# Performance work log

Hardware: AMD Instinct MI355X
Metric: run time of the kernel (lower is better)

The kernel has to match this reference:

```python
import jax, jax.numpy as jnp
import numpy as np

BATCH_SIZE = 8192   # args.batch_size
NUM_VIEWS = 2       # args.num_views
TEMPERATURE = 0.07  # args.loss_args['temperature']
FEAT_DIM = 256
N = (BATCH_SIZE // 2) * NUM_VIEWS  # rows of features


def _static_index_maps():
    # labels = sorted cat of num_views copies of arange(batch_size//2)
    labels = np.sort(np.tile(np.arange(BATCH_SIZE // 2), NUM_VIEWS))
    lab_mat = labels[None, :] == labels[:, None]          # (N, N) bool
    # off-diagonal column indices: for row i, columns [0..N-1] excluding i,
    # in ascending order (matches torch boolean-mask extraction order)
    j = np.arange(N - 1)
    cols = j[None, :] + (j[None, :] >= np.arange(N)[:, None])  # (N, N-1)
    lab_off = np.take_along_axis(lab_mat, cols, axis=1)        # (N, N-1) bool
    k = NUM_VIEWS - 1  # positives per row
    # stable sort puts positive positions first, preserving column order
    order = np.argsort(~lab_off, axis=1, kind='stable')
    pos_cols = order[:, :k]   # (N, k)
    neg_cols = order[:, k:]   # (N, N-1-k)
    return cols, pos_cols, neg_cols

_COLS, _POS_COLS, _NEG_COLS = _static_index_maps()


def setup_inputs() -> dict:
    key = jax.random.key(0)
    features = jax.random.normal(key, (N, FEAT_DIM), dtype=jnp.float32)
    return {"features": features}


def reference(features):
    # L2 normalize rows (F.normalize eps clamp)
    norm = jnp.maximum(jnp.linalg.norm(features, axis=1, keepdims=True), 1e-12)
    f = features / norm
    sim = f @ f.T                                            # (N, N)
    sim_off = jnp.take_along_axis(sim, jnp.asarray(_COLS), axis=1)       # (N, N-1)
    positives = jnp.take_along_axis(sim_off, jnp.asarray(_POS_COLS), axis=1)
    negatives = jnp.take_along_axis(sim_off, jnp.asarray(_NEG_COLS), axis=1)
    logits = jnp.concatenate([positives, negatives], axis=1) / TEMPERATURE
    # CrossEntropyLoss with target class 0 for every row
    loss = jnp.mean(-jax.nn.log_softmax(logits, axis=1)[:, 0])
    return loss
```

## Files before the change

### kernel.cpp

```cpp
#include <hip/hip_runtime.h>
#include <stdint.h>

#define N_ROWS 8192
#define FEAT   256
#define YSPLIT 16
#define CPB    (N_ROWS / YSPLIT)
#define CT     64
#define LDS_STRIDE 264

typedef __bf16 bf16x8 __attribute__((ext_vector_type(8)));
typedef float  f32x4  __attribute__((ext_vector_type(4)));

__device__ __forceinline__ unsigned short f2bf(float x) {
    union { float f; uint32_t u; } v; v.f = x;
    uint32_t u = v.u;
    return (unsigned short)((u + 0x7FFFu + ((u >> 16) & 1u)) >> 16);
}

__global__ void knorm(const float* __restrict__ feat,
                      unsigned short* __restrict__ fb,
                      float* __restrict__ pos) {
    __shared__ float ex[4][FEAT];
    int wave = threadIdx.x >> 6;
    int lane = threadIdx.x & 63;
    int row  = blockIdx.x * 4 + wave;
    float4 v = ((const float4*)(feat + row * FEAT))[lane];
    float ss = v.x*v.x + v.y*v.y + v.z*v.z + v.w*v.w;
    #pragma unroll
    for (int off = 1; off < 64; off <<= 1) ss += __shfl_xor(ss, off);
    float inv = 1.0f / fmaxf(sqrtf(ss), 1e-12f);
    float4 o; o.x = v.x*inv; o.y = v.y*inv; o.z = v.z*inv; o.w = v.w*inv;
    ushort4 b;
    b.x = f2bf(o.x); b.y = f2bf(o.y); b.z = f2bf(o.z); b.w = f2bf(o.w);
    ((ushort4*)(fb + row * FEAT))[lane] = b;
    ((float4*)ex[wave])[lane] = o;
    __syncthreads();
    float4 p = ((float4*)ex[wave ^ 1])[lane];
    float d = o.x*p.x + o.y*p.y + o.z*p.z + o.w*p.w;
    #pragma unroll
    for (int off = 1; off < 64; off <<= 1) d += __shfl_xor(d, off);
    if (lane == 0) pos[row] = d;
}

__global__ __launch_bounds__(512)
void kmain(const unsigned short* __restrict__ fb, float* __restrict__ partial) {
    __shared__ unsigned short Bs[CT][LDS_STRIDE];
    const int t    = threadIdx.x;
    const int lane = t & 63;
    const int wave = t >> 6;
    const int quad = lane >> 4;
    const int l15  = lane & 15;
    const int rw    = blockIdx.x * 256 + wave * 32;
    const int cbase = blockIdx.y * CPB;
    const float Kc = 20.60992915555662f;

    bf16x8 af[2][8];
    #pragma unroll
    for (int rf = 0; rf < 2; ++rf)
        #pragma unroll
        for (int ks = 0; ks < 8; ++ks) {
            int row = rw + rf * 16 + l15;
            int k   = ks * 32 + quad * 8;
            af[rf][ks] = *(const bf16x8*)(fb + row * FEAT + k);
        }

    float lsum[2][4] = {{0.f,0.f,0.f,0.f},{0.f,0.f,0.f,0.f}};

    for (int ct = 0; ct < CPB / CT; ++ct) {
        __syncthreads();
        const int c0 = cbase + ct * CT;
        #pragma unroll
        for (int i = 0; i < 4; ++i) {
            int idx = t + i * 512;
            int r = idx >> 5;
            int o = (idx & 31) * 8;
            *(uint4*)(&Bs[r][o]) = *(const uint4*)(fb + (c0 + r) * FEAT + o);
        }
        __syncthreads();

        #pragma unroll
        for (int g = 0; g < 4; ++g) {
            const int cg = c0 + g * 16;
            f32x4 acc0 = {0.f,0.f,0.f,0.f};
            f32x4 acc1 = {0.f,0.f,0.f,0.f};
            #pragma unroll
            for (int ks = 0; ks < 8; ++ks) {
                bf16x8 b = *(const bf16x8*)(&Bs[g * 16 + l15][ks * 32 + quad * 8]);
                acc0 = __builtin_amdgcn_mfma_f32_16x16x32_bf16(af[0][ks], b, acc0, 0, 0, 0);
                acc1 = __builtin_amdgcn_mfma_f32_16x16x32_bf16(af[1][ks], b, acc1, 0, 0, 0);
            }
            const bool dg = (cg < rw + 32) && (cg + 16 > rw);
            const int C = cg + l15;
            #pragma unroll
            for (int r = 0; r < 4; ++r) {
                float e0 = __builtin_amdgcn_exp2f(fmaf(acc0[r], Kc, -Kc));
                float e1 = __builtin_amdgcn_exp2f(fmaf(acc1[r], Kc, -Kc));
                if (dg) {
                    int R0 = rw + quad * 4 + r;
                    if (R0 == C)      e0 = 0.f;
                    if (R0 + 16 == C) e1 = 0.f;
                }
                lsum[0][r] += e0;
                lsum[1][r] += e1;
            }
        }
    }

    #pragma unroll
    for (int rf = 0; rf < 2; ++rf)
        #pragma unroll
        for (int r = 0; r < 4; ++r) {
            float v = lsum[rf][r];
            v += __shfl_xor(v, 1);
            v += __shfl_xor(v, 2);
            v += __shfl_xor(v, 4);
            v += __shfl_xor(v, 8);
            lsum[rf][r] = v;
        }
    if (l15 == 0) {
        #pragma unroll
        for (int rf = 0; rf < 2; ++rf)
            #pragma unroll
            for (int r = 0; r < 4; ++r) {
                int row = rw + rf * 16 + quad * 4 + r;
                partial[blockIdx.y * N_ROWS + row] = lsum[rf][r];
            }
    }
}

__global__ void kreduce(const float* __restrict__ partial,
                        const float* __restrict__ pos,
                        float* __restrict__ bsum) {
    __shared__ float red[4];
    int row  = blockIdx.x * 256 + threadIdx.x;
    int wave = threadIdx.x >> 6;
    int lane = threadIdx.x & 63;
    float L = 0.f;
    #pragma unroll
    for (int p = 0; p < YSPLIT; ++p) L += partial[p * N_ROWS + row];
    const float invT = 14.285714285714286f;
    float loss = invT * (1.0f - pos[row])
               + 0.6931471805599453f * __builtin_amdgcn_logf(L);
    #pragma unroll
    for (int off = 1; off < 64; off <<= 1) loss += __shfl_xor(loss, off);
    if (lane == 0) red[wave] = loss;
    __syncthreads();
    if (threadIdx.x == 0)
        bsum[blockIdx.x] = red[0] + red[1] + red[2] + red[3];
}

__global__ void kfinal(const float* __restrict__ bsum, float* __restrict__ out) {
    int lane = threadIdx.x;
    float v = (lane < 32) ? bsum[lane] : 0.f;
    #pragma unroll
    for (int off = 1; off < 32; off <<= 1) v += __shfl_xor(v, off);
    if (lane == 0) out[0] = v * (1.0f / 8192.0f);
}

extern "C" void kernel_launch(void* const* d_in, const int* in_sizes, int n_in,
                              void* d_out, int out_size, void* d_ws, size_t ws_size,
                              hipStream_t stream) {
    const float* feat = (const float*)d_in[0];
    float* out = (float*)d_out;
    char* ws = (char*)d_ws;
    unsigned short* fb      = (unsigned short*)ws;
    float*          partial = (float*)(ws + (4u << 20));
    float*          pos     = (float*)(ws + (4u << 20) + (1u << 19));
    float*          bsum    = (float*)(ws + (4u << 20) + (1u << 19) + (1u << 15));

    knorm<<<N_ROWS / 4, 256, 0, stream>>>(feat, fb, pos);
    kmain<<<dim3(32, YSPLIT), 512, 0, stream>>>(fb, partial);
    kreduce<<<N_ROWS / 256, 256, 0, stream>>>(partial, pos, bsum);
    kfinal<<<1, 64, 0, stream>>>(bsum, out);
}
```

Before: 104.8 us.

## Double-buffer B tiles via direct global-to-LDS loads with swizzled layout

The main kernel now stages column tiles straight from global memory into LDS with global_load_lds, using two buffers so the next tile loads while the current one is computed. The normalize kernel writes bf16 rows in an XOR-swizzled chunk order, which lets the unpadded LDS tile avoid bank conflicts. Each wave now handles 64 rows instead of 32, with 256 threads per block and launch bounds requesting two blocks per CU, so each LDS B fragment feeds four MFMAs. This costs more registers for the A fragments and accumulators, and the LDS footprint doubles.

After: 125.4 us. 19.7% more time.

```diff
diff --git a/kernel.cpp b/kernel.cpp
--- a/kernel.cpp
+++ b/kernel.cpp
@@ -6,7 +6,6 @@
 #define YSPLIT 16
 #define CPB    (N_ROWS / YSPLIT)
 #define CT     64
-#define LDS_STRIDE 264
 
 typedef __bf16 bf16x8 __attribute__((ext_vector_type(8)));
 typedef float  f32x4  __attribute__((ext_vector_type(4)));
@@ -15,6 +14,12 @@
     union { float f; uint32_t u; } v; v.f = x;
     uint32_t u = v.u;
     return (unsigned short)((u + 0x7FFFu + ((u >> 16) & 1u)) >> 16);
+}
+
+__device__ __forceinline__ void gld16(const unsigned short* g, unsigned short* l) {
+    __builtin_amdgcn_global_load_lds((__attribute__((address_space(1))) void*)g,
+                                     (__attribute__((address_space(3))) void*)l,
+                                     16, 0, 0);
 }
 
 __global__ void knorm(const float* __restrict__ feat,
@@ -32,7 +37,8 @@
     float4 o; o.x = v.x*inv; o.y = v.y*inv; o.z = v.z*inv; o.w = v.w*inv;
     ushort4 b;
     b.x = f2bf(o.x); b.y = f2bf(o.y); b.z = f2bf(o.z); b.w = f2bf(o.w);
-    ((ushort4*)(fb + row * FEAT))[lane] = b;
+    int sidx = (((lane >> 1) ^ (row & 7)) << 1) | (lane & 1);
+    ((ushort4*)(fb + row * FEAT))[sidx] = b;
     ((float4*)ex[wave])[lane] = o;
     __syncthreads();
     float4 p = ((float4*)ex[wave ^ 1])[lane];
@@ -42,72 +48,90 @@
     if (lane == 0) pos[row] = d;
 }
 
-__global__ __launch_bounds__(512)
+__global__ __launch_bounds__(256, 2)
 void kmain(const unsigned short* __restrict__ fb, float* __restrict__ partial) {
-    __shared__ unsigned short Bs[CT][LDS_STRIDE];
+    __shared__ unsigned short bufA[CT * FEAT];
+    __shared__ unsigned short bufB[CT * FEAT];
     const int t    = threadIdx.x;
     const int lane = t & 63;
     const int wave = t >> 6;
     const int quad = lane >> 4;
     const int l15  = lane & 15;
-    const int rw    = blockIdx.x * 256 + wave * 32;
+    const int rw    = blockIdx.x * 256 + wave * 64;
     const int cbase = blockIdx.y * CPB;
     const float Kc = 20.60992915555662f;
 
-    bf16x8 af[2][8];
-    #pragma unroll
-    for (int rf = 0; rf < 2; ++rf)
+#define STAGE(DST, CC0) do {                                                  \
+    const unsigned short* sp_ = fb + (size_t)(cbase + (CC0)) * FEAT + t * 8;  \
+    unsigned short* dp_ = (DST) + t * 8;                                      \
+    _Pragma("unroll")                                                         \
+    for (int i_ = 0; i_ < 8; ++i_)                                            \
+        gld16(sp_ + i_ * 2048, dp_ + i_ * 2048);                              \
+} while (0)
+
+    STAGE(bufA, 0);
+
+    bf16x8 af[4][8];
+    #pragma unroll
+    for (int rf = 0; rf < 4; ++rf)
         #pragma unroll
         for (int ks = 0; ks < 8; ++ks) {
             int row = rw + rf * 16 + l15;
-            int k   = ks * 32 + quad * 8;
-            af[rf][ks] = *(const bf16x8*)(fb + row * FEAT + k);
+            int ch  = (ks * 4 + quad) ^ (row & 7);
+            af[rf][ks] = *(const bf16x8*)(fb + row * FEAT + ch * 8);
         }
 
-    float lsum[2][4] = {{0.f,0.f,0.f,0.f},{0.f,0.f,0.f,0.f}};
-
-    for (int ct = 0; ct < CPB / CT; ++ct) {
-        __syncthreads();
-        const int c0 = cbase + ct * CT;
-        #pragma unroll
-        for (int i = 0; i < 4; ++i) {
-            int idx = t + i * 512;
-            int r = idx >> 5;
-            int o = (idx & 31) * 8;
-            *(uint4*)(&Bs[r][o]) = *(const uint4*)(fb + (c0 + r) * FEAT + o);
-        }
-        __syncthreads();
-
-        #pragma unroll
-        for (int g = 0; g < 4; ++g) {
-            const int cg = c0 + g * 16;
-            f32x4 acc0 = {0.f,0.f,0.f,0.f};
-            f32x4 acc1 = {0.f,0.f,0.f,0.f};
-            #pragma unroll
-            for (int ks = 0; ks < 8; ++ks) {
-                bf16x8 b = *(const bf16x8*)(&Bs[g * 16 + l15][ks * 32 + quad * 8]);
-                acc0 = __builtin_amdgcn_mfma_f32_16x16x32_bf16(af[0][ks], b, acc0, 0, 0, 0);
-                acc1 = __builtin_amdgcn_mfma_f32_16x16x32_bf16(af[1][ks], b, acc1, 0, 0, 0);
-            }
-            const bool dg = (cg < rw + 32) && (cg + 16 > rw);
-            const int C = cg + l15;
-            #pragma unroll
-            for (int r = 0; r < 4; ++r) {
-                float e0 = __builtin_amdgcn_exp2f(fmaf(acc0[r], Kc, -Kc));
-                float e1 = __builtin_amdgcn_exp2f(fmaf(acc1[r], Kc, -Kc));
-                if (dg) {
-                    int R0 = rw + quad * 4 + r;
-                    if (R0 == C)      e0 = 0.f;
-                    if (R0 + 16 == C) e1 = 0.f;
-                }
-                lsum[0][r] += e0;
-                lsum[1][r] += e1;
-            }
-        }
+    float lsum[4][4] = {{0.f,0.f,0.f,0.f},{0.f,0.f,0.f,0.f},
+                        {0.f,0.f,0.f,0.f},{0.f,0.f,0.f,0.f}};
+
+#define EPI(AC, RF) do {                                                      \
+    const int rb_ = rw + (RF) * 16;                                           \
+    const bool dg_ = (cg == rb_);          \
+    _Pragma("unroll")                                                         \
+    for (int r_ = 0; r_ < 4; ++r_) {                                          \
+        float e_ = __builtin_amdgcn_exp2f(fmaf((AC)[r_], Kc, -Kc));           \
+        if (dg_ && (rb_ + quad * 4 + r_ == C)) e_ = 0.f;     \
+        lsum[(RF)][r_] += e_;                                                 \
+    }                                                                         \
+} while (0)
+
+#define COMPUTE(BS, CC0) do {                                                 \
+    _Pragma("unroll")                                                         \
+    for (int g = 0; g < 4; ++g) {                                             \
+        const int cg = cbase + (CC0) + g * 16;                                \
+        const int C  = cg + l15;                                              \
+        f32x4 ac0 = {0.f,0.f,0.f,0.f};                                        \
+        f32x4 ac1 = {0.f,0.f,0.f,0.f};                                        \
+        f32x4 ac2 = {0.f,0.f,0.f,0.f};                                        \
+        f32x4 ac3 = {0.f,0.f,0.f,0.f};                                        \
+        _Pragma("unroll")                                                     \
+        for (int ks = 0; ks < 8; ++ks) {                                      \
+            bf16x8 b = *(const bf16x8*)((BS) + (g * 16 + l15) * FEAT          \
+                                        + (((ks * 4 + quad) ^ (l15 & 7)) * 8)); \
+            ac0 = __builtin_amdgcn_mfma_f32_16x16x32_bf16(af[0][ks], b, ac0, 0, 0, 0); \
+            ac1 = __builtin_amdgcn_mfma_f32_16x16x32_bf16(af[1][ks], b, ac1, 0, 0, 0); \
+            ac2 = __builtin_amdgcn_mfma_f32_16x16x32_bf16(af[2][ks], b, ac2, 0, 0, 0); \
+            ac3 = __builtin_amdgcn_mfma_f32_16x16x32_bf16(af[3][ks], b, ac3, 0, 0, 0); \
+        }                                                                     \
+        EPI(ac0, 0); EPI(ac1, 1); EPI(ac2, 2); EPI(ac3, 3);                   \
+    }                                                                         \
+} while (0)
+
+    asm volatile("s_waitcnt vmcnt(0)" ::: "memory");
+    __builtin_amdgcn_s_barrier();
+    for (int ct2 = 0; ct2 < CPB / CT; ct2 += 2) {
+        STAGE(bufB, (ct2 + 1) * CT);
+        COMPUTE(bufA, ct2 * CT);
+        asm volatile("s_waitcnt vmcnt(0)" ::: "memory");
+        __builtin_amdgcn_s_barrier();
+        if (ct2 + 2 < CPB / CT) STAGE(bufA, (ct2 + 2) * CT);
+        COMPUTE(bufB, (ct2 + 1) * CT);
+        asm volatile("s_waitcnt vmcnt(0)" ::: "memory");
+        __builtin_amdgcn_s_barrier();
     }
 
     #pragma unroll
-    for (int rf = 0; rf < 2; ++rf)
+    for (int rf = 0; rf < 4; ++rf)
         #pragma unroll
         for (int r = 0; r < 4; ++r) {
             float v = lsum[rf][r];
@@ -119,13 +143,16 @@
         }
     if (l15 == 0) {
         #pragma unroll
-        for (int rf = 0; rf < 2; ++rf)
+        for (int rf = 0; rf < 4; ++rf)
             #pragma unroll
             for (int r = 0; r < 4; ++r) {
                 int row = rw + rf * 16 + quad * 4 + r;
                 partial[blockIdx.y * N_ROWS + row] = lsum[rf][r];
             }
     }
+#undef STAGE
+#undef COMPUTE
+#undef EPI
 }
 
 __global__ void kreduce(const float* __restrict__ partial,
@@ -169,7 +196,7 @@
     float*          bsum    = (float*)(ws + (4u << 20) + (1u << 19) + (1u << 15));
 
     knorm<<<N_ROWS / 4, 256, 0, stream>>>(feat, fb, pos);
-    kmain<<<dim3(32, YSPLIT), 512, 0, stream>>>(fb, partial);
+    kmain<<<dim3(32, YSPLIT), 256, 0, stream>>>(fb, partial);
     kreduce<<<N_ROWS / 256, 256, 0, stream>>>(partial, pos, bsum);
     kfinal<<<1, 64, 0, stream>>>(bsum, out);
 }
```

## Drop LDS staging; read B fragments directly from swizzled global bf16 layout

Applied to the files above, without the earlier changes.

The normalize kernel now writes bf16 rows with an XOR swizzle of 16-byte chunks keyed by row. The main kernel drops the shared-memory tile and its barriers and loads B fragments straight from global memory or L2 using the matching swizzle. Each wave now covers 64 rows instead of 32, with 4 accumulators per B load, and blocks shrink to 256 threads. This removes LDS traffic and synchronisation and reuses each B fragment twice as much. The cost is higher register pressure, lower occupancy, and exposed global-load latency.

After: 106.0 us. Within noise of the previous version (+1.2%).

```diff
diff --git a/kernel.cpp b/kernel.cpp
--- a/kernel.cpp
+++ b/kernel.cpp
@@ -5,8 +5,6 @@
 #define FEAT   256
 #define YSPLIT 16
 #define CPB    (N_ROWS / YSPLIT)
-#define CT     64
-#define LDS_STRIDE 264
 
 typedef __bf16 bf16x8 __attribute__((ext_vector_type(8)));
 typedef float  f32x4  __attribute__((ext_vector_type(4)));
@@ -32,7 +30,8 @@
     float4 o; o.x = v.x*inv; o.y = v.y*inv; o.z = v.z*inv; o.w = v.w*inv;
     ushort4 b;
     b.x = f2bf(o.x); b.y = f2bf(o.y); b.z = f2bf(o.z); b.w = f2bf(o.w);
-    ((ushort4*)(fb + row * FEAT))[lane] = b;
+    int sidx = (((lane >> 1) ^ (row & 7)) << 1) | (lane & 1);
+    ((ushort4*)(fb + row * FEAT))[sidx] = b;
     ((float4*)ex[wave])[lane] = o;
     __syncthreads();
     float4 p = ((float4*)ex[wave ^ 1])[lane];
@@ -42,72 +41,64 @@
     if (lane == 0) pos[row] = d;
 }
 
-__global__ __launch_bounds__(512)
+__global__ __launch_bounds__(256, 1)
 void kmain(const unsigned short* __restrict__ fb, float* __restrict__ partial) {
-    __shared__ unsigned short Bs[CT][LDS_STRIDE];
     const int t    = threadIdx.x;
     const int lane = t & 63;
     const int wave = t >> 6;
     const int quad = lane >> 4;
     const int l15  = lane & 15;
-    const int rw    = blockIdx.x * 256 + wave * 32;
+    const int rw    = blockIdx.x * 256 + wave * 64;
     const int cbase = blockIdx.y * CPB;
     const float Kc = 20.60992915555662f;
 
-    bf16x8 af[2][8];
+    bf16x8 af[4][8];
     #pragma unroll
-    for (int rf = 0; rf < 2; ++rf)
+    for (int rf = 0; rf < 4; ++rf)
         #pragma unroll
         for (int ks = 0; ks < 8; ++ks) {
             int row = rw + rf * 16 + l15;
-            int k   = ks * 32 + quad * 8;
-            af[rf][ks] = *(const bf16x8*)(fb + row * FEAT + k);
+            int ch  = (ks * 4 + quad) ^ (row & 7);
+            af[rf][ks] = *(const bf16x8*)(fb + row * FEAT + ch * 8);
         }
 
-    float lsum[2][4] = {{0.f,0.f,0.f,0.f},{0.f,0.f,0.f,0.f}};
+    float lsum[4][4] = {{0.f,0.f,0.f,0.f},{0.f,0.f,0.f,0.f},
+                        {0.f,0.f,0.f,0.f},{0.f,0.f,0.f,0.f}};
 
-    for (int ct = 0; ct < CPB / CT; ++ct) {
-        __syncthreads();
-        const int c0 = cbase + ct * CT;
+    #pragma unroll 2
+    for (int g = 0; g < CPB / 16; ++g) {
+        const int cg = cbase + g * 16;
+        const int C  = cg + l15;
+        const unsigned short* bp = fb + (size_t)(cg + l15) * FEAT;
+        f32x4 ac0 = {0.f,0.f,0.f,0.f};
+        f32x4 ac1 = {0.f,0.f,0.f,0.f};
+        f32x4 ac2 = {0.f,0.f,0.f,0.f};
+        f32x4 ac3 = {0.f,0.f,0.f,0.f};
         #pragma unroll
-        for (int i = 0; i < 4; ++i) {
-            int idx = t + i * 512;
-            int r = idx >> 5;
-            int o = (idx & 31) * 8;
-            *(uint4*)(&Bs[r][o]) = *(const uint4*)(fb + (c0 + r) * FEAT + o);
+        for (int ks = 0; ks < 8; ++ks) {
+            bf16x8 bv = *(const bf16x8*)(bp + (((ks * 4 + quad) ^ (l15 & 7)) * 8));
+            ac0 = __builtin_amdgcn_mfma_f32_16x16x32_bf16(af[0][ks], bv, ac0, 0, 0, 0);
+            ac1 = __builtin_amdgcn_mfma_f32_16x16x32_bf16(af[1][ks], bv, ac1, 0, 0, 0);
+            ac2 = __builtin_amdgcn_mfma_f32_16x16x32_bf16(af[2][ks], bv, ac2, 0, 0, 0);
+            ac3 = __builtin_amdgcn_mfma_f32_16x16x32_bf16(af[3][ks], bv, ac3, 0, 0, 0);
         }
-        __syncthreads();
-
         #pragma unroll
-        for (int g = 0; g < 4; ++g) {
-            const int cg = c0 + g * 16;
-            f32x4 acc0 = {0.f,0.f,0.f,0.f};
-            f32x4 acc1 = {0.f,0.f,0.f,0.f};
-            #pragma unroll
-            for (int ks = 0; ks < 8; ++ks) {
-                bf16x8 b = *(const bf16x8*)(&Bs[g * 16 + l15][ks * 32 + quad * 8]);
-                acc0 = __builtin_amdgcn_mfma_f32_16x16x32_bf16(af[0][ks], b, acc0, 0, 0, 0);
-                acc1 = __builtin_amdgcn_mfma_f32_16x16x32_bf16(af[1][ks], b, acc1, 0, 0, 0);
-            }
-            const bool dg = (cg < rw + 32) && (cg + 16 > rw);
-            const int C = cg + l15;
+        for (int rf = 0; rf < 4; ++rf) {
+            const int rb = rw + rf * 16;
+            const bool dg = (cg == rb);
+            const f32x4 ac = (rf == 0) ? ac0 : (rf == 1) ? ac1
+                           : (rf == 2) ? ac2 : ac3;
             #pragma unroll
             for (int r = 0; r < 4; ++r) {
-                float e0 = __builtin_amdgcn_exp2f(fmaf(acc0[r], Kc, -Kc));
-                float e1 = __builtin_amdgcn_exp2f(fmaf(acc1[r], Kc, -Kc));
-                if (dg) {
-                    int R0 = rw + quad * 4 + r;
-                    if (R0 == C)      e0 = 0.f;
-                    if (R0 + 16 == C) e1 = 0.f;
-                }
-                lsum[0][r] += e0;
-                lsum[1][r] += e1;
+                float e = __builtin_amdgcn_exp2f(fmaf(ac[r], Kc, -Kc));
+                if (dg && (rb + quad * 4 + r == C)) e = 0.f;
+                lsum[rf][r] += e;
             }
         }
     }
 
     #pragma unroll
-    for (int rf = 0; rf < 2; ++rf)
+    for (int rf = 0; rf < 4; ++rf)
         #pragma unroll
         for (int r = 0; r < 4; ++r) {
             float v = lsum[rf][r];
@@ -119,7 +110,7 @@
         }
     if (l15 == 0) {
         #pragma unroll
-        for (int rf = 0; rf < 2; ++rf)
+        for (int rf = 0; rf < 4; ++rf)
             #pragma unroll
             for (int r = 0; r < 4; ++r) {
                 int row = rw + rf * 16 + quad * 4 + r;
@@ -169,7 +160,7 @@
     float*          bsum    = (float*)(ws + (4u << 20) + (1u << 19) + (1u << 15));
 
     knorm<<<N_ROWS / 4, 256, 0, stream>>>(feat, fb, pos);
-    kmain<<<dim3(32, YSPLIT), 512, 0, stream>>>(fb, partial);
+    kmain<<<dim3(32, YSPLIT), 256, 0, stream>>>(fb, partial);
     kreduce<<<N_ROWS / 256, 256, 0, stream>>>(partial, pos, bsum);
     kfinal<<<1, 64, 0, stream>>>(bsum, out);
 }
```
